# Kernel tuning notes

Measured on AMD Instinct MI355X. Metric: run time of the kernel, lower is better.

## Reference

```python
import jax, jax.numpy as jnp
import numpy as np

N_NODES = 100000
N_EDGES = 500000
FEAT = 128
HID = 256
N_ETYPES = 249
N_LINKS = 16384


def _lin_init(key, out_dim, in_dim, bias=True):
    k1, k2 = jax.random.split(key)
    bound = 1.0 / np.sqrt(in_dim)
    w = jax.random.uniform(k1, (out_dim, in_dim), jnp.float32, -bound, bound)
    if bias:
        b = jax.random.uniform(k2, (out_dim,), jnp.float32, -bound, bound)
        return w, b
    return w


def setup_inputs() -> dict:
    key = jax.random.key(0)
    ks = jax.random.split(key, 24)
    x = jax.random.normal(ks[0], (N_NODES, FEAT), jnp.float32)
    edge_index = jax.random.randint(ks[1], (2, N_EDGES), 0, N_NODES, jnp.int64)
    edge_type = jax.random.randint(ks[2], (N_EDGES,), 0, N_ETYPES, jnp.int64)
    src_idx = jax.random.randint(ks[3], (N_LINKS,), 0, N_NODES, jnp.int64)
    dst_idx = jax.random.randint(ks[4], (N_LINKS,), 0, N_NODES, jnp.int64)

    w_emb, b_emb = _lin_init(ks[5], HID, FEAT)
    edge_table = jax.random.normal(ks[6], (N_ETYPES, HID), jnp.float32)
    wl0, bl0 = _lin_init(ks[7], HID, HID)
    wr0 = _lin_init(ks[8], HID, HID, bias=False)
    we0, be0 = _lin_init(ks[9], HID, HID)
    wl1, bl1 = _lin_init(ks[10], HID, HID)
    wr1 = _lin_init(ks[11], HID, HID, bias=False)
    we1, be1 = _lin_init(ks[12], HID, HID)
    wp1, bp1 = _lin_init(ks[13], HID, 4 * HID)
    wp2, bp2 = _lin_init(ks[14], 1, HID)
    return dict(x=x, edge_index=edge_index, edge_type=edge_type,
                src_idx=src_idx, dst_idx=dst_idx,
                w_emb=w_emb, b_emb=b_emb, edge_table=edge_table,
                wl0=wl0, bl0=bl0, wr0=wr0, we0=we0, be0=be0,
                wl1=wl1, bl1=bl1, wr1=wr1, we1=we1, be1=be1,
                wp1=wp1, bp1=bp1, wp2=wp2, bp2=bp2)


def _sage_layer(h, src, dst, deg, wl, bl, wr):
    # mean aggregation over incoming edges + self loop (add_self_loops)
    nb_sum = jax.ops.segment_sum(h[src], dst, num_segments=N_NODES)  # [N,H]
    mean = (nb_sum + h) / (deg + 1.0)[:, None]
    return mean @ wl.T + bl + h @ wr.T  # lin_l(mean) + lin_r(x)


def reference(x, edge_index, edge_type, src_idx, dst_idx,
              w_emb, b_emb, edge_table,
              wl0, bl0, wr0, we0, be0,
              wl1, bl1, wr1, we1, be1,
              wp1, bp1, wp2, bp2):
    src, dst = edge_index[0], edge_index[1]
    deg = jax.ops.segment_sum(jnp.ones((src.shape[0],), jnp.float32), dst,
                              num_segments=N_NODES)  # in-degree (no self loop)
    h = x @ w_emb.T + b_emb  # node_embedding
    edge_emb = edge_table[edge_type]  # [E,H]
    # edge_lin outputs are discarded by SAGEConv (matches torch behavior)
    _ = edge_emb @ we0.T + be0
    _ = edge_emb @ we1.T + be1
    h = jax.nn.relu(_sage_layer(h, src, dst, deg, wl0, bl0, wr0))
    h = jax.nn.relu(_sage_layer(h, src, dst, deg, wl1, bl1, wr1))
    s, d = h[src_idx], h[dst_idx]
    combined = jnp.concatenate([s, d, s * d, jnp.abs(s - d)], axis=1)  # [B,4H]
    hidden = jax.nn.relu(combined @ wp1.T + bp1)
    logits = hidden @ wp2.T + bp2  # [B,1]
    return jax.nn.sigmoid(logits).squeeze()
```

## Files before the change

kernel.cpp:

```cpp
#include <hip/hip_runtime.h>
#include <hip/hip_bf16.h>
#include <cstdint>
#include <type_traits>

#define N_NODES 100000
#define N_EDGES 500000
#define FEAT 128
#define HID 256
#define N_LINKS 16384
#define BCAP 32

typedef __attribute__((ext_vector_type(8))) short short8;
typedef __attribute__((ext_vector_type(4))) float floatx4;
typedef __attribute__((ext_vector_type(16))) float floatx16;

__device__ __forceinline__ float ldf(const float* p) { return *p; }
__device__ __forceinline__ float ldf(const __hip_bfloat16* p) { return __bfloat162float(*p); }
__device__ __forceinline__ void stf(float* p, float v) { *p = v; }
__device__ __forceinline__ void stf(__hip_bfloat16* p, float v) { *p = __float2bfloat16(v); }

__device__ __forceinline__ void load4(const __hip_bfloat16* p, float v[4]) {
    const uint2 q = *(const uint2*)p;
    v[0] = __uint_as_float(q.x << 16);
    v[1] = __uint_as_float(q.x & 0xffff0000u);
    v[2] = __uint_as_float(q.y << 16);
    v[3] = __uint_as_float(q.y & 0xffff0000u);
}
__device__ __forceinline__ void store4(__hip_bfloat16* p, const float v[4]) {
    __hip_bfloat16 b[4];
    b[0] = __float2bfloat16(v[0]); b[1] = __float2bfloat16(v[1]);
    b[2] = __float2bfloat16(v[2]); b[3] = __float2bfloat16(v[3]);
    *(uint2*)p = *(const uint2*)b;
}

__device__ __forceinline__ void load8(const __hip_bfloat16* p, float v[8]) {
    const uint4 q = *(const uint4*)p;
    v[0] = __uint_as_float(q.x << 16);
    v[1] = __uint_as_float(q.x & 0xffff0000u);
    v[2] = __uint_as_float(q.y << 16);
    v[3] = __uint_as_float(q.y & 0xffff0000u);
    v[4] = __uint_as_float(q.z << 16);
    v[5] = __uint_as_float(q.z & 0xffff0000u);
    v[6] = __uint_as_float(q.w << 16);
    v[7] = __uint_as_float(q.w & 0xffff0000u);
}
__device__ __forceinline__ void store8(__hip_bfloat16* p, const float v[8]) {
    __hip_bfloat16 b[8];
    #pragma unroll
    for (int i = 0; i < 8; i++) b[i] = __float2bfloat16(v[i]);
    *(uint4*)p = *(const uint4*)b;
}

__device__ __forceinline__ void acc8(const uint4& q, float a[8]) {
    a[0] += __uint_as_float(q.x << 16);
    a[1] += __uint_as_float(q.x & 0xffff0000u);
    a[2] += __uint_as_float(q.y << 16);
    a[3] += __uint_as_float(q.y & 0xffff0000u);
    a[4] += __uint_as_float(q.z << 16);
    a[5] += __uint_as_float(q.z & 0xffff0000u);
    a[6] += __uint_as_float(q.w << 16);
    a[7] += __uint_as_float(q.w & 0xffff0000u);
}

__device__ __forceinline__ void gload_lds16(const short* g, short* lds) {
    __builtin_amdgcn_global_load_lds(
        reinterpret_cast<const __attribute__((address_space(1))) unsigned int*>(
            reinterpret_cast<uintptr_t>(g)),
        reinterpret_cast<__attribute__((address_space(3))) unsigned int*>(
            reinterpret_cast<uintptr_t>(lds)),
        16, 0, 0);
}

__device__ __forceinline__ int clampi(int v, int n) { return ((unsigned)v < (unsigned)n) ? v : 0; }


__global__ void zero_f32(float* p, int n) {
    int i = blockIdx.x * blockDim.x + threadIdx.x;
    if (i < n) p[i] = 0.0f;
}

__global__ void init_misc(int* __restrict__ deg, int* __restrict__ h0pad,
                          int* __restrict__ h1pad) {
    int i = blockIdx.x * blockDim.x + threadIdx.x;
    if (i < N_NODES) deg[i] = 0;
    if (i < 128) { h0pad[i] = 0; h1pad[i] = 0; }
}

__global__ void cvt_x(const float4* __restrict__ x, __hip_bfloat16* __restrict__ xb, int n4) {
    int i = blockIdx.x * blockDim.x + threadIdx.x;
    if (i >= n4) return;
    float4 v = x[i];
    float a[4] = {v.x, v.y, v.z, v.w};
    store4(&xb[(size_t)i * 4], a);
}

#define POF_EMB 0
#define POF_L0  32768
#define POF_R0  98304
#define POF_L1  163840
#define POF_R1  229376
#define POF_P1  294912
#define WP_ALL  557056
__global__ void cvt_wall(const float* __restrict__ w_emb, const float* __restrict__ wl0,
                         const float* __restrict__ wr0, const float* __restrict__ wl1,
                         const float* __restrict__ wr1, const float* __restrict__ wp1,
                         __hip_bfloat16* __restrict__ wbp) {
    int i = blockIdx.x * blockDim.x + threadIdx.x;
    if (i >= WP_ALL) return;
    const float* src; int off, ks;
    if      (i < POF_L0) { src = w_emb; off = POF_EMB; ks = 128; }
    else if (i < POF_R0) { src = wl0;   off = POF_L0;  ks = 256; }
    else if (i < POF_L1) { src = wr0;   off = POF_R0;  ks = 256; }
    else if (i < POF_R1) { src = wl1;   off = POF_L1;  ks = 256; }
    else if (i < POF_P1) { src = wr1;   off = POF_R1;  ks = 256; }
    else                 { src = wp1;   off = POF_P1;  ks = 1024; }
    int o = i - off;
    int kseg = o >> 11;
    int rem  = o & 2047;
    int n = rem >> 3, j = rem & 7;
    wbp[i] = __float2bfloat16(src[n * ks + kseg * 8 + j]);
}


__global__ void fill_buckets(const int* __restrict__ src, const int* __restrict__ dst,
                             int* __restrict__ deg, int* __restrict__ ebuf, int nE) {
    int e = blockIdx.x * blockDim.x + threadIdx.x;
    if (e >= nE) return;
    int d = clampi(dst[e], N_NODES);
    int pos = atomicAdd(&deg[d], 1);
    if (pos < BCAP) ebuf[d * BCAP + pos] = clampi(src[e], N_NODES);
}

__global__ void sort_rows(const int* __restrict__ deg, int* __restrict__ ebuf) {
    int n = blockIdx.x * blockDim.x + threadIdx.x;
    if (n >= N_NODES) return;
    int dg = deg[n]; if (dg > BCAP) dg = BCAP;
    int start = n * BCAP, end = start + dg;
    for (int i = start + 1; i < end; i++) {
        int key = ebuf[i];
        int j = i - 1;
        while (j >= start && ebuf[j] > key) { ebuf[j + 1] = ebuf[j]; j--; }
        ebuf[j + 1] = key;
    }
}


__global__ __launch_bounds__(256) void gather_agg(const __hip_bfloat16* __restrict__ h,
                                                  const int* __restrict__ deg,
                                                  const int* __restrict__ ebuf,
                                                  __hip_bfloat16* __restrict__ agg) {
    int wave = threadIdx.x >> 6, lane = threadIdx.x & 63;
    int half = lane >> 5, l32 = lane & 31;
    int n = blockIdx.x * 8 + wave * 2 + half;
    bool active = (n < N_NODES);
    int nn = active ? n : 0;
    int dg = active ? deg[nn] : 0;
    int dgc = dg > BCAP ? BCAP : dg;
    int start = nn * BCAP;
    int end = start + dgc;

    float acc[8];
    {
        float sv[8];
        load8(&h[(long long)nn * HID + l32 * 8], sv);
        #pragma unroll
        for (int k = 0; k < 8; k++) acc[k] = sv[k];
    }

    for (int e = start; e < end; e += 8) {
        int cnt = end - e;
        uint4 raw[8];
        #pragma unroll
        for (int i = 0; i < 8; i++) {
            int t = e + i; t = (t < end) ? t : (end - 1);
            int idx = ebuf[t];
            int s = (i < cnt) ? idx : N_NODES;
            raw[i] = *(const uint4*)&h[(long long)s * HID + l32 * 8];
        }
        #pragma unroll
        for (int i = 0; i < 8; i++) acc8(raw[i], acc);
    }

    float inv = 1.0f / (float)(dg + 1);
    #pragma unroll
    for (int k = 0; k < 8; k++) acc[k] *= inv;
    if (active) store8(&agg[(long long)n * HID + l32 * 8], acc);
}


template <int KS, bool DUAL, typename TC, bool RELU>
__global__ __launch_bounds__(256, 2) void gemm_kc(const __hip_bfloat16* __restrict__ A1,
                                                  const __hip_bfloat16* __restrict__ A2,
                                                  const __hip_bfloat16* __restrict__ Bp1,
                                                  const __hip_bfloat16* __restrict__ Bp2,
                                                  const float* __restrict__ bias,
                                                  TC* __restrict__ C, int M, int GX) {
    const int N = 256;
    const int NSTEP = (DUAL ? 2 : 1) * KS / 64;
    __shared__ __align__(16) short As[2][128 * 64];
    __shared__ __align__(16) short Bs[2][64 * 128];

    const int tid = threadIdx.x;
    const int w = tid >> 6, lane = tid & 63;
    const int half = lane >> 5, l32 = lane & 31;
    const int cg = blockIdx.y;

    const short* A1s = (const short*)A1;
    const short* A2s = (const short*)A2;
    const short* B1s = (const short*)Bp1;
    const short* B2s = (const short*)Bp2;

    const int NT = (M + 127) / 128;
    for (int tile = blockIdx.x; tile < NT; tile += GX) {
        const int row0 = tile * 128;

        auto stage = [&](int buf, int t) {
            const short* Asrc; const short* Bsrc; int kl;
            if (!DUAL || t < KS / 64) { Asrc = A1s; Bsrc = B1s; kl = t * 64; }
            else                      { Asrc = A2s; Bsrc = B2s; kl = t * 64 - KS; }
            #pragma unroll
            for (int i = 0; i < 4; i++) {
                int idx = i * 256 + tid;
                int row = idx >> 3, b16 = idx & 7;
                int gr = row0 + row; if (gr >= M) gr = M - 1;
                gload_lds16(Asrc + (size_t)gr * KS + kl + ((b16 ^ (row & 7)) * 8),
                            (short*)&As[buf][idx * 8]);
            }
            #pragma unroll
            for (int i = 0; i < 4; i++) {
                int idx = i * 256 + tid;
                int kseg = idx >> 7, col = idx & 127;
                gload_lds16(Bsrc + ((size_t)((kl >> 3) + kseg) * 256 + cg * 128 + col) * 8,
                            (short*)&Bs[buf][idx * 8]);
            }
        };

        floatx16 acc[4] = {};
        int cur = 0;
        stage(0, 0);
        __syncthreads();

        for (int t = 0; t < NSTEP; t++) {
            if (t + 1 < NSTEP) stage(cur ^ 1, t + 1);

            const int arow = w * 32 + l32;
            #pragma unroll
            for (int k16 = 0; k16 < 4; k16++) {
                int e = k16 * 2 + half;
                short8 a = *(const short8*)&As[cur][(arow * 8 + (e ^ (l32 & 7))) * 8];
                #pragma unroll
                for (int ct = 0; ct < 4; ct++) {
                    short8 b = *(const short8*)&Bs[cur][(e * 128 + ct * 32 + l32) * 8];
                    acc[ct] = __builtin_amdgcn_mfma_f32_32x32x16_bf16(a, b, acc[ct], 0, 0, 0);
                }
            }
            __syncthreads();
            cur ^= 1;
        }

        #pragma unroll
        for (int ct = 0; ct < 4; ct++) {
            int c = cg * 128 + ct * 32 + l32;
            float bc = bias[c];
            #pragma unroll
            for (int reg = 0; reg < 16; reg++) {
                int rr = row0 + w * 32 + (reg & 3) + 8 * (reg >> 2) + 4 * half;
                if (rr < M) {
                    float v = acc[ct][reg] + bc;
                    if (RELU) v = fmaxf(v, 0.0f);
                    stf(&C[(size_t)rr * N + c], v);
                }
            }
        }
    }
}


__device__ __forceinline__ short8 comb_frag(const __hip_bfloat16* __restrict__ h,
                                            int srow, int drow, int ka) {
    int seg = ka >> 8, off = ka & 255;
    const __hip_bfloat16* ps = &h[(size_t)srow * HID + off];
    const __hip_bfloat16* pd = &h[(size_t)drow * HID + off];
    if (seg == 0) return *(const short8*)ps;
    if (seg == 1) return *(const short8*)pd;
    float s[8], d[8];
    load8(ps, s);
    load8(pd, d);
    __hip_bfloat16 b[8];
    if (seg == 2) {
        #pragma unroll
        for (int j = 0; j < 8; j++) b[j] = __float2bfloat16(s[j] * d[j]);
    } else {
        #pragma unroll
        for (int j = 0; j < 8; j++) b[j] = __float2bfloat16(fabsf(s[j] - d[j]));
    }
    return *(const short8*)b;
}


__global__ __launch_bounds__(256, 4) void pred_gemm(const __hip_bfloat16* __restrict__ h,
                                                    const int* __restrict__ src_idx,
                                                    const int* __restrict__ dst_idx,
                                                    const __hip_bfloat16* __restrict__ Bp,
                                                    const float* __restrict__ bias,
                                                    float* __restrict__ C, int M) {
    const int N = 256;
    const int K = 1024;
    __shared__ __align__(16) short Bs[2][4 * 64 * 8];

    int w = threadIdx.x >> 6, lane = threadIdx.x & 63;
    int quad = lane >> 4, l16 = lane & 15;
    int cg = blockIdx.y;
    int row0 = blockIdx.x * 64 + w * 16;

    const short* Bps = (const short*)Bp;

    floatx4 acc[4] = {};

    int rr = row0 + l16;
    int r = rr < M ? rr : M - 1;
    int sidx = clampi(src_idx[r], N_NODES);
    int didx = clampi(dst_idx[r], N_NODES);

    auto stageB = [&](int buf, int k0) {
        gload_lds16(Bps + ((size_t)((k0 >> 3) + w) * 256 + cg * 64 + lane) * 8,
                    (short*)&Bs[buf][(w * 64 + lane) * 8]);
    };

    short8 a1c, a1n;
    stageB(0, 0);
    a1c = comb_frag(h, sidx, didx, quad * 8);
    __syncthreads();

    const int NK = K / 32;
    int cur = 0;
    for (int k = 0; k < NK; k++) {
        if (k + 1 < NK) {
            stageB(cur ^ 1, (k + 1) * 32);
            a1n = comb_frag(h, sidx, didx, (k + 1) * 32 + quad * 8);
        }
        #pragma unroll
        for (int ct = 0; ct < 4; ct++) {
            short8 b = *(const short8*)&Bs[cur][(quad * 64 + ct * 16 + l16) * 8];
            acc[ct] = __builtin_amdgcn_mfma_f32_16x16x32_bf16(a1c, b, acc[ct], 0, 0, 0);
        }
        __syncthreads();
        cur ^= 1;
        a1c = a1n;
    }

    #pragma unroll
    for (int ct = 0; ct < 4; ct++) {
        int c = cg * 64 + ct * 16 + l16;
        float bc = bias[c];
        #pragma unroll
        for (int i = 0; i < 4; i++) {
            int r2 = row0 + quad * 4 + i;
            if (r2 < M) C[(size_t)r2 * N + c] = fmaxf(acc[ct][i] + bc, 0.0f);
        }
    }
}

__global__ __launch_bounds__(256) void pred_final(const float* __restrict__ hidden,
                                                  const float* __restrict__ wp2,
                                                  const float* __restrict__ bp2,
                                                  float* __restrict__ out) {
    int wave = threadIdx.x >> 6;
    int lane = threadIdx.x & 63;
    int row = blockIdx.x * 4 + wave;
    if (row >= N_LINKS) return;
    const float4 hv = *(const float4*)&hidden[(long long)row * HID + lane * 4];
    const float4 wv = *(const float4*)&wp2[lane * 4];
    float v = hv.x * wv.x + hv.y * wv.y + hv.z * wv.z + hv.w * wv.w;
    #pragma unroll
    for (int off = 32; off > 0; off >>= 1) v += __shfl_down(v, off, 64);
    if (lane == 0) out[row] = 1.0f / (1.0f + expf(-(v + bp2[0])));
}


extern "C" void kernel_launch(void* const* d_in, const int* in_sizes, int n_in,
                              void* d_out, int out_size, void* d_ws, size_t ws_size,
                              hipStream_t stream) {
    const float* x          = (const float*)d_in[0];
    const int*   edge_index = (const int*)d_in[1];
    const int*   e_src      = edge_index;
    const int*   e_dst      = edge_index + N_EDGES;
    const int*   src_idx    = (const int*)d_in[3];
    const int*   dst_idx    = (const int*)d_in[4];
    const float* w_emb      = (const float*)d_in[5];
    const float* b_emb      = (const float*)d_in[6];
    const float* wl0        = (const float*)d_in[8];
    const float* bl0        = (const float*)d_in[9];
    const float* wr0        = (const float*)d_in[10];
    const float* wl1        = (const float*)d_in[13];
    const float* bl1        = (const float*)d_in[14];
    const float* wr1        = (const float*)d_in[15];
    const float* wp1        = (const float*)d_in[18];
    const float* bp1        = (const float*)d_in[19];
    const float* wp2        = (const float*)d_in[20];
    const float* bp2        = (const float*)d_in[21];
    float* out = (float*)d_out;

    typedef __hip_bfloat16 bf16;
    const size_t NH  = (size_t)N_NODES * HID;
    const size_t NH1 = (size_t)(N_NODES + 1) * HID;

    char* p = (char*)d_ws;
    bf16* h0   = (bf16*)p;  p += NH1 * 2;
    bf16* h1   = (bf16*)p;  p += NH1 * 2;
    bf16* agg  = (bf16*)p;  p += NH * 2;
    bf16* xb   = (bf16*)p;  p += (size_t)N_NODES * FEAT * 2;
    bf16* wbp  = (bf16*)p;  p += (size_t)WP_ALL * 2;
    p = (char*)(((uintptr_t)p + 255) & ~(uintptr_t)255);
    int* deg  = (int*)p; p += (size_t)N_NODES * 4;
    int* ebuf = (int*)p; p += (size_t)N_NODES * BCAP * 4;
    const size_t need = (size_t)(p - (char*)d_ws);

    if (ws_size < need) {
        zero_f32<<<(out_size + 255) / 256, 256, 0, stream>>>(out, out_size);
        return;
    }

    float* hidden = (float*)h1;

    init_misc<<<(N_NODES + 255) / 256, 256, 0, stream>>>(
        deg, (int*)(h0 + NH), (int*)(h1 + NH));
    fill_buckets<<<(N_EDGES + 255) / 256, 256, 0, stream>>>(e_src, e_dst, deg, ebuf, N_EDGES);
    sort_rows<<<(N_NODES + 255) / 256, 256, 0, stream>>>(deg, ebuf);

    cvt_x<<<((N_NODES * FEAT / 4) + 255) / 256, 256, 0, stream>>>((const float4*)x, xb, N_NODES * FEAT / 4);
    cvt_wall<<<(WP_ALL + 255) / 256, 256, 0, stream>>>(
        w_emb, wl0, wr0, wl1, wr1, wp1, wbp);

    const int GX = 256;
    dim3 pgrid(GX, 2);

    gemm_kc<128, false, bf16, false><<<pgrid, 256, 0, stream>>>(
        xb, nullptr, wbp + POF_EMB, nullptr, b_emb, h0, N_NODES, GX);

    gather_agg<<<(N_NODES + 7) / 8, 256, 0, stream>>>(h0, deg, ebuf, agg);
    gemm_kc<256, true, bf16, true><<<pgrid, 256, 0, stream>>>(
        agg, h0, wbp + POF_L0, wbp + POF_R0, bl0, h1, N_NODES, GX);

    gather_agg<<<(N_NODES + 7) / 8, 256, 0, stream>>>(h1, deg, ebuf, agg);
    gemm_kc<256, true, bf16, true><<<pgrid, 256, 0, stream>>>(
        agg, h1, wbp + POF_L1, wbp + POF_R1, bl1, h0, N_NODES, GX);

    dim3 pgrid2(N_LINKS / 64, 4);
    pred_gemm<<<pgrid2, 256, 0, stream>>>(
        h0, src_idx, dst_idx, wbp + POF_P1, bp1, hidden, N_LINKS);
    pred_final<<<N_LINKS / 4, 256, 0, stream>>>(hidden, wp2, bp2, out);
}
```

Before: 468.3 us.

## Preload link src/dst rows into registers and stage B in larger K chunks

The link-prediction GEMM now loads each row's full source and destination embeddings into registers once, instead of re-gathering them from global memory every K step. The concat features (s, d, s*d, |s-d|) are built from those registers. B tiles are staged 128 K-values at a time, which cuts the main loop from 32 barriers to 8. The cost is more register pressure and four times the LDS, with launch bounds lowered from 4 to 3 blocks per SM.

After: 436.4 us. -6.8%, faster.

```diff
diff --git a/kernel.cpp b/kernel.cpp
--- a/kernel.cpp
+++ b/kernel.cpp
@@ -49,6 +49,17 @@
     #pragma unroll
     for (int i = 0; i < 8; i++) b[i] = __float2bfloat16(v[i]);
     *(uint4*)p = *(const uint4*)b;
+}
+
+__device__ __forceinline__ void unpack8(const uint4& q, float v[8]) {
+    v[0] = __uint_as_float(q.x << 16);
+    v[1] = __uint_as_float(q.x & 0xffff0000u);
+    v[2] = __uint_as_float(q.y << 16);
+    v[3] = __uint_as_float(q.y & 0xffff0000u);
+    v[4] = __uint_as_float(q.z << 16);
+    v[5] = __uint_as_float(q.z & 0xffff0000u);
+    v[6] = __uint_as_float(q.w << 16);
+    v[7] = __uint_as_float(q.w & 0xffff0000u);
 }
 
 __device__ __forceinline__ void acc8(const uint4& q, float a[8]) {
@@ -276,37 +287,14 @@
 }
 
 
-__device__ __forceinline__ short8 comb_frag(const __hip_bfloat16* __restrict__ h,
-                                            int srow, int drow, int ka) {
-    int seg = ka >> 8, off = ka & 255;
-    const __hip_bfloat16* ps = &h[(size_t)srow * HID + off];
-    const __hip_bfloat16* pd = &h[(size_t)drow * HID + off];
-    if (seg == 0) return *(const short8*)ps;
-    if (seg == 1) return *(const short8*)pd;
-    float s[8], d[8];
-    load8(ps, s);
-    load8(pd, d);
-    __hip_bfloat16 b[8];
-    if (seg == 2) {
-        #pragma unroll
-        for (int j = 0; j < 8; j++) b[j] = __float2bfloat16(s[j] * d[j]);
-    } else {
-        #pragma unroll
-        for (int j = 0; j < 8; j++) b[j] = __float2bfloat16(fabsf(s[j] - d[j]));
-    }
-    return *(const short8*)b;
-}
-
-
-__global__ __launch_bounds__(256, 4) void pred_gemm(const __hip_bfloat16* __restrict__ h,
+__global__ __launch_bounds__(256, 3) void pred_gemm(const __hip_bfloat16* __restrict__ h,
                                                     const int* __restrict__ src_idx,
                                                     const int* __restrict__ dst_idx,
                                                     const __hip_bfloat16* __restrict__ Bp,
                                                     const float* __restrict__ bias,
                                                     float* __restrict__ C, int M) {
     const int N = 256;
-    const int K = 1024;
-    __shared__ __align__(16) short Bs[2][4 * 64 * 8];
+    __shared__ __align__(16) short Bs[2][16 * 64 * 8];
 
     int w = threadIdx.x >> 6, lane = threadIdx.x & 63;
     int quad = lane >> 4, l16 = lane & 15;
@@ -315,38 +303,67 @@
 
     const short* Bps = (const short*)Bp;
 
-    floatx4 acc[4] = {};
-
     int rr = row0 + l16;
     int r = rr < M ? rr : M - 1;
     int sidx = clampi(src_idx[r], N_NODES);
     int didx = clampi(dst_idx[r], N_NODES);
 
-    auto stageB = [&](int buf, int k0) {
-        gload_lds16(Bps + ((size_t)((k0 >> 3) + w) * 256 + cg * 64 + lane) * 8,
-                    (short*)&Bs[buf][(w * 64 + lane) * 8]);
+    uint4 sraw[8], draw[8];
+    #pragma unroll
+    for (int j = 0; j < 8; j++) {
+        sraw[j] = *(const uint4*)&h[(size_t)sidx * HID + quad * 8 + j * 32];
+        draw[j] = *(const uint4*)&h[(size_t)didx * HID + quad * 8 + j * 32];
+    }
+
+    auto stageB = [&](int buf, int chunk) {
+        #pragma unroll
+        for (int i = 0; i < 4; i++) {
+            int idx = i * 256 + (int)threadIdx.x;
+            int ks = idx >> 6, col = idx & 63;
+            gload_lds16(Bps + ((size_t)(chunk * 16 + ks) * 256 + cg * 64 + col) * 8,
+                        (short*)&Bs[buf][idx * 8]);
+        }
     };
 
-    short8 a1c, a1n;
+    floatx4 acc[4] = {};
     stageB(0, 0);
-    a1c = comb_frag(h, sidx, didx, quad * 8);
     __syncthreads();
-
-    const int NK = K / 32;
     int cur = 0;
-    for (int k = 0; k < NK; k++) {
-        if (k + 1 < NK) {
-            stageB(cur ^ 1, (k + 1) * 32);
-            a1n = comb_frag(h, sidx, didx, (k + 1) * 32 + quad * 8);
-        }
-        #pragma unroll
-        for (int ct = 0; ct < 4; ct++) {
-            short8 b = *(const short8*)&Bs[cur][(quad * 64 + ct * 16 + l16) * 8];
-            acc[ct] = __builtin_amdgcn_mfma_f32_16x16x32_bf16(a1c, b, acc[ct], 0, 0, 0);
+
+    #pragma unroll
+    for (int c = 0; c < 8; c++) {
+        if (c + 1 < 8) stageB(cur ^ 1, c + 1);
+
+        #pragma unroll
+        for (int s = 0; s < 4; s++) {
+            const int j = ((c & 1) ? 4 : 0) + s;
+            short8 a;
+            if (c < 2) {
+                a = *(const short8*)&sraw[j];
+            } else if (c < 4) {
+                a = *(const short8*)&draw[j];
+            } else {
+                float sv[8], dv[8];
+                unpack8(sraw[j], sv);
+                unpack8(draw[j], dv);
+                __hip_bfloat16 b8[8];
+                if (c < 6) {
+                    #pragma unroll
+                    for (int q = 0; q < 8; q++) b8[q] = __float2bfloat16(sv[q] * dv[q]);
+                } else {
+                    #pragma unroll
+                    for (int q = 0; q < 8; q++) b8[q] = __float2bfloat16(fabsf(sv[q] - dv[q]));
+                }
+                a = *(const short8*)b8;
+            }
+            #pragma unroll
+            for (int ct = 0; ct < 4; ct++) {
+                short8 b = *(const short8*)&Bs[cur][((s * 4 + quad) * 64 + ct * 16 + l16) * 8];
+                acc[ct] = __builtin_amdgcn_mfma_f32_16x16x32_bf16(a, b, acc[ct], 0, 0, 0);
+            }
         }
         __syncthreads();
         cur ^= 1;
-        a1c = a1n;
     }
 
     #pragma unroll
```
